# Optimization experiments

Hardware: AMD Instinct MI355X
Metric: run time of the kernel (lower is better)

Reference implementation:

```python
import jax, jax.numpy as jnp
import numpy as np

N, M, D, O = 16384, 4096, 256, 256

def setup_inputs() -> dict:
    key = jax.random.key(0)
    k1, k2, k3, k4, k5, k6, k7 = jax.random.split(key, 7)
    H_fine = jax.random.normal(k1, (N, D), dtype=jnp.float32)
    H_coarse = jax.random.normal(k2, (M, D), dtype=jnp.float32)
    inter_channel_adj = jax.random.randint(k3, (N, M), 0, 2).astype(jnp.float32)
    # attention = nn.Linear(2D, 1): weight vector [2D], bias scalar
    wa = jax.random.normal(k4, (2 * D,), dtype=jnp.float32) * (1.0 / np.sqrt(2 * D))
    ba = jax.random.normal(k5, (1,), dtype=jnp.float32) * 0.01
    # transform = nn.Linear(D, O), xavier_uniform weight
    lim = np.sqrt(6.0 / (D + O)).astype(np.float32)
    Wt = jax.random.uniform(k6, (O, D), minval=-lim, maxval=lim, dtype=jnp.float32)
    bt = jax.random.normal(k7, (O,), dtype=jnp.float32) * 0.01
    return {"H_fine": H_fine, "H_coarse": H_coarse,
            "inter_channel_adj": inter_channel_adj,
            "wa": wa, "ba": ba, "Wt": Wt, "bt": bt}

def reference(H_fine, H_coarse, inter_channel_adj, wa, ba, Wt, bt):
    d = H_fine.shape[-1]
    # additive attention: score_ij = [hf_i ; hc_j] . wa + b
    # = hf_i . wa[:d] + hc_j . wa[d:] + b  (avoids [N,M,2D] concat)
    sf = H_fine @ wa[:d]            # [N]
    sc = H_coarse @ wa[d:]          # [M]
    scores = sf[:, None] + sc[None, :] + ba[0]        # [N, M]
    masked = scores * inter_channel_adj               # [N, M]
    weights = jax.nn.softmax(masked, axis=-1)         # [N, M]
    attn_out = weights @ H_coarse                     # [N, D]
    attn_out = attn_out + H_fine                      # add_self=True
    out = attn_out @ Wt.T + bt                        # [N, O]
    return jax.nn.relu(out)
```

## Files before the change

kernel.cpp:

```cpp
#include <hip/hip_runtime.h>
#include <hip/hip_fp16.h>
#include <stdint.h>

#define N_ 16384
#define M_ 4096
#define D_ 256
#define O_ 256

#define WS_T    0
#define WS_U    65536
#define WS_R    81920
#define WS_WTP  98304
#define WS_BP   229376

typedef float  f32x4  __attribute__((ext_vector_type(4)));
typedef _Float16 half8 __attribute__((ext_vector_type(8)));

__device__ __forceinline__ unsigned short f2h(float f) {
  __half h = __float2half(f);
  unsigned short u;
  __builtin_memcpy(&u, &h, 2);
  return u;
}
__device__ __forceinline__ uint32_t hpack(float a, float b) {
  __half2 h = __floats2half2_rn(a, b);
  uint32_t u;
  __builtin_memcpy(&u, &h, 4);
  return u;
}

__global__ __launch_bounds__(256) void prep_kernel(
    const float* __restrict__ Hf, const float* __restrict__ Hc,
    const float* __restrict__ wa, const float* __restrict__ ba,
    const float* __restrict__ Wt, float* __restrict__ tv,
    float* __restrict__ uv, unsigned short* __restrict__ BP,
    unsigned short* __restrict__ WtP, float* __restrict__ Rv) {
  __shared__ float tile[64][65];
  __shared__ float red[4][64];
  int b = blockIdx.x;
  int t = threadIdx.x;
  if (b < 5120) {
    int wv = t >> 6, lane = t & 63;
    const float* X; const float* w; const float* bias; float* outv; int row;
    if (b < 4096) { X = Hf; w = wa;      bias = ba;      outv = tv; row = b * 4 + wv; }
    else          { X = Hc; w = wa + D_; bias = nullptr; outv = uv; row = (b - 4096) * 4 + wv; }
    const float4* x4 = (const float4*)(X + (size_t)row * D_);
    const float4* w4 = (const float4*)w;
    float4 xa = x4[lane], wa4 = w4[lane];
    float s = xa.x * wa4.x + xa.y * wa4.y + xa.z * wa4.z + xa.w * wa4.w;
#pragma unroll
    for (int off = 32; off > 0; off >>= 1) s += __shfl_xor(s, off);
    if (lane == 0) outv[row] = expf(s + (bias ? bias[0] : 0.0f));
  } else if (b < 5376) {
    int bb = b - 5120;
    int bk = bb >> 2;
    int bc = bb & 3;
    int k0 = bk * 64, col0 = bc * 64;
    int lane = t & 63, wv = t >> 6;
    int m = lane & 15, q = lane >> 4;
    float colsum = 0.0f;
#pragma unroll
    for (int i = 0; i < 16; ++i) {
      int e = t + 256 * i;
      int kk = e >> 6, cc = e & 63;
      float v = Hc[(size_t)(k0 + kk) * D_ + col0 + cc];
      tile[kk][cc] = v;
      colsum += v;
    }
    red[wv][t & 63] = colsum;
    __syncthreads();
    if (t < 64)
      atomicAdd(&Rv[col0 + t], red[0][t] + red[1][t] + red[2][t] + red[3][t]);
#pragma unroll
    for (int t8 = 0; t8 < 2; ++t8) {
      int tile_id = t8 * 4 + wv;
      int sub = tile_id >> 2, g = tile_id & 3;
      int kgg = bk * 2 + sub;
      int cgg = bc * 4 + g;
      unsigned short v8[8];
#pragma unroll
      for (int j = 0; j < 8; ++j)
        v8[j] = f2h(tile[sub * 32 + q * 8 + j][g * 16 + m]);
      *(uint4*)(BP + ((size_t)(kgg * 16 + cgg) * 64 + lane) * 8) = *(uint4*)v8;
    }
  } else {
    int tt = (b - 5376) * 256 + t;
    int lane = tt & 63, cg = (tt >> 6) & 15, kg = tt >> 10;
    int m = lane & 15, q = lane >> 4;
    const float* src = Wt + (size_t)(cg * 16 + m) * D_ + kg * 32 + q * 8;
    float4 w0 = *(const float4*)src, w1 = *(const float4*)(src + 4);
    unsigned short v8[8];
    v8[0] = f2h(w0.x); v8[1] = f2h(w0.y); v8[2] = f2h(w0.z); v8[3] = f2h(w0.w);
    v8[4] = f2h(w1.x); v8[5] = f2h(w1.y); v8[6] = f2h(w1.z); v8[7] = f2h(w1.w);
    *(uint4*)(WtP + (size_t)tt * 8) = *(uint4*)v8;
  }
}

__device__ __forceinline__ half8 frag_f16(uint32_t bits, __half2 th,
                                          const __half2* up, __half2 mone) {
  union { half8 h; uint32_t u[4]; } r;
#pragma unroll
  for (int p = 0; p < 4; ++p) {
    __half2 v = __hfma2(th, up[p], mone);
    uint32_t c;
    __builtin_memcpy(&c, &v, 4);
    uint32_t mlo = (uint32_t)((int32_t)(bits << (31 - 2 * p)) >> 31);
    uint32_t mhi = (uint32_t)((int32_t)(bits << (30 - 2 * p)) >> 31);
    r.u[p] = c & ((mlo & 0x0000FFFFu) | (mhi & 0xFFFF0000u));
  }
  return r.h;
}

#define LOADS(KB)                                                             \
  _Pragma("unroll")                                                           \
  for (int cc = 0; cc < 4; ++cc) {                                            \
    na0[cc] = ar[(size_t)0 * M_ + (KB) + cc * 64 + lane];                     \
    na1[cc] = ar[(size_t)1 * M_ + (KB) + cc * 64 + lane];                     \
    na2[cc] = ar[(size_t)2 * M_ + (KB) + cc * 64 + lane];                     \
    na3[cc] = ar[(size_t)3 * M_ + (KB) + cc * 64 + lane];                     \
  }

#define TAIL(BUF, KB)                                                         \
  {                                                                           \
    unsigned long long bal0[4], bal1[4], bal2[4], bal3[4];                    \
    _Pragma("unroll")                                                         \
    for (int cc = 0; cc < 4; ++cc) {                                          \
      float uvv = u_lds[(KB) + cc * 64 + lane];                               \
      bal0[cc] = __ballot(na0[cc] != 0.0f);                                   \
      bal1[cc] = __ballot(na1[cc] != 0.0f);                                   \
      bal2[cc] = __ballot(na2[cc] != 0.0f);                                   \
      bal3[cc] = __ballot(na3[cc] != 0.0f);                                   \
      su[0] = fmaf(na0[cc], uvv, su[0]);                                      \
      su[1] = fmaf(na1[cc], uvv, su[1]);                                      \
      su[2] = fmaf(na2[cc], uvv, su[2]);                                      \
      su[3] = fmaf(na3[cc], uvv, su[3]);                                      \
    }                                                                         \
    sc[0] += (na0[0] + na0[1]) + (na0[2] + na0[3]);                           \
    sc[1] += (na1[0] + na1[1]) + (na1[2] + na1[3]);                           \
    sc[2] += (na2[0] + na2[1]) + (na2[2] + na2[3]);                           \
    sc[3] += (na3[0] + na3[1]) + (na3[2] + na3[3]);                           \
    if (lane < 32) {                                                          \
      int rowsel = lane >> 3, ccs = (lane >> 1) & 3, hi = lane & 1;           \
      unsigned long long v0 = ccs == 0 ? bal0[0] : ccs == 1 ? bal0[1] : ccs == 2 ? bal0[2] : bal0[3]; \
      unsigned long long v1 = ccs == 0 ? bal1[0] : ccs == 1 ? bal1[1] : ccs == 2 ? bal1[2] : bal1[3]; \
      unsigned long long v2 = ccs == 0 ? bal2[0] : ccs == 1 ? bal2[1] : ccs == 2 ? bal2[2] : bal2[3]; \
      unsigned long long v3 = ccs == 0 ? bal3[0] : ccs == 1 ? bal3[1] : ccs == 2 ? bal3[2] : bal3[3]; \
      unsigned long long v = rowsel == 0 ? v0 : rowsel == 1 ? v1 : rowsel == 2 ? v2 : v3; \
      bits_lds[BUF][w * 4 + rowsel][ccs * 2 + hi] =                           \
          hi ? (unsigned int)(v >> 32) : (unsigned int)v;                     \
    }                                                                         \
  }

#define COMPUTE(C, BUF)                                                       \
  _Pragma("unroll")                                                           \
  for (int kk = 0; kk < 4; ++kk) {                                            \
    int kgc = ks * 4 + kk, kg = (C) * 8 + kgc;                                \
    uint32_t b32 = bits_lds[BUF][rt * 16 + m][kgc];                           \
    uint4 uu = *(const uint4*)&u_h2[kg * 16 + q * 4];                         \
    const unsigned short* bp = BP + ((size_t)(kg * 16 + cgh * 8)) * 512 + (size_t)lane * 8; \
    half8 bf0 = *(const half8*)(bp);                                          \
    half8 bf1 = *(const half8*)(bp + 512);                                    \
    half8 bf2 = *(const half8*)(bp + 1024);                                   \
    half8 bf3 = *(const half8*)(bp + 1536);                                   \
    half8 bf4 = *(const half8*)(bp + 2048);                                   \
    half8 bf5 = *(const half8*)(bp + 2560);                                   \
    half8 bf6 = *(const half8*)(bp + 3072);                                   \
    half8 bf7 = *(const half8*)(bp + 3584);                                   \
    __half2 up[4];                                                            \
    __builtin_memcpy(up, &uu, 16);                                            \
    half8 af = frag_f16((b32 >> sh) & 0xffu, th, up, mone);                   \
    acc[0] = __builtin_amdgcn_mfma_f32_16x16x32_f16(af, bf0, acc[0], 0, 0, 0); \
    acc[1] = __builtin_amdgcn_mfma_f32_16x16x32_f16(af, bf1, acc[1], 0, 0, 0); \
    acc[2] = __builtin_amdgcn_mfma_f32_16x16x32_f16(af, bf2, acc[2], 0, 0, 0); \
    acc[3] = __builtin_amdgcn_mfma_f32_16x16x32_f16(af, bf3, acc[3], 0, 0, 0); \
    acc[4] = __builtin_amdgcn_mfma_f32_16x16x32_f16(af, bf4, acc[4], 0, 0, 0); \
    acc[5] = __builtin_amdgcn_mfma_f32_16x16x32_f16(af, bf5, acc[5], 0, 0, 0); \
    acc[6] = __builtin_amdgcn_mfma_f32_16x16x32_f16(af, bf6, acc[6], 0, 0, 0); \
    acc[7] = __builtin_amdgcn_mfma_f32_16x16x32_f16(af, bf7, acc[7], 0, 0, 0); \
  }

__global__ __launch_bounds__(512, 4) void mega_kernel(
    const float* __restrict__ adj, const unsigned short* __restrict__ BP,
    const float* __restrict__ tv, const float* __restrict__ uv,
    const float* __restrict__ Rv, const float* __restrict__ Hf,
    const unsigned short* __restrict__ WtP, const float* __restrict__ bt,
    float* __restrict__ out) {
  __shared__ __align__(16) char smem[60288];
  unsigned int (*bits_lds)[32][9] = (unsigned int (*)[32][9])(smem);
  float* u_lds = (float*)(smem + 2304);
  uint32_t* u_h2 = (uint32_t*)(smem + 18688);
  float (*Cred)[260] = (float (*)[260])(smem + 26880);
  float* Lsum_lds = (float*)(smem + 60160);
  unsigned short (*attn)[264] = (unsigned short (*)[264])(smem);

  int tid = threadIdx.x;
  int w = tid >> 6, lane = tid & 63;
  int q = lane >> 4, m = lane & 15;
  int rt = w & 1, cgh = (w >> 1) & 1, ks = w >> 2;
  int sh = q * 8;
  int i0 = blockIdx.x * 32;

  const float* ar = adj + ((size_t)i0 + w * 4) * M_;
  float su[4] = {0.f, 0.f, 0.f, 0.f}, sc[4] = {0.f, 0.f, 0.f, 0.f};
  float na0[4], na1[4], na2[4], na3[4];

  LOADS(0)

  for (int i = tid; i < M_ / 2; i += 512) {
    float2 u2 = *(const float2*)(uv + 2 * i);
    u_lds[2 * i] = u2.x; u_lds[2 * i + 1] = u2.y;
    u_h2[i] = hpack(u2.x, u2.y);
  }

  __half2 th = __float2half2_rn(tv[i0 + rt * 16 + m]);
  const __half2 mone = __float2half2_rn(-1.0f);

  f32x4 acc[8];
#pragma unroll
  for (int n = 0; n < 8; ++n) acc[n] = (f32x4){0.f, 0.f, 0.f, 0.f};

  __syncthreads();
  TAIL(0, 0)
  __syncthreads();

#pragma unroll 1
  for (int c = 0; c < 16; ++c) {
    if (c < 15) { LOADS((c + 1) * 256) }
    COMPUTE(c, c & 1)
    if (c < 15) { TAIL((c + 1) & 1, (c + 1) * 256) }
    __syncthreads();
  }

#pragma unroll
  for (int off = 32; off > 0; off >>= 1) {
    su[0] += __shfl_xor(su[0], off); sc[0] += __shfl_xor(sc[0], off);
    su[1] += __shfl_xor(su[1], off); sc[1] += __shfl_xor(sc[1], off);
    su[2] += __shfl_xor(su[2], off); sc[2] += __shfl_xor(sc[2], off);
    su[3] += __shfl_xor(su[3], off); sc[3] += __shfl_xor(sc[3], off);
  }
  if (lane == 0) {
#pragma unroll
    for (int j = 0; j < 4; ++j)
      Lsum_lds[w * 4 + j] = tv[i0 + w * 4 + j] * su[j] - sc[j];
  }

#pragma unroll
  for (int s4 = 0; s4 < 2; ++s4) {
    if (ks == s4) {
#pragma unroll
      for (int g = 0; g < 8; ++g) {
        int col = (cgh * 8 + g) * 16 + m;
#pragma unroll
        for (int r = 0; r < 4; ++r) {
          int rl = rt * 16 + q * 4 + r;
          if (s4 == 0) Cred[rl][col] = acc[g][r];
          else         Cred[rl][col] += acc[g][r];
        }
      }
    }
    __syncthreads();
  }

  {
    int row = tid >> 4;
    int c0 = (tid & 15) * 16;
    size_t grow = (size_t)i0 + row;
    float invL = 1.0f / (Lsum_lds[row] + (float)M_);
    const float* hfp = Hf + grow * D_ + c0;
    const float* rvp = Rv + c0;
    const float* crp = &Cred[row][c0];
#pragma unroll
    for (int g = 0; g < 4; ++g) {
      float4 cv = *(const float4*)(crp + g * 4);
      float4 rv = *(const float4*)(rvp + g * 4);
      float4 hv = *(const float4*)(hfp + g * 4);
      float v0 = fmaf(cv.x + rv.x, invL, hv.x);
      float v1 = fmaf(cv.y + rv.y, invL, hv.y);
      float v2 = fmaf(cv.z + rv.z, invL, hv.z);
      float v3 = fmaf(cv.w + rv.w, invL, hv.w);
      *(uint32_t*)&attn[row][c0 + g * 4]     = hpack(v0, v1);
      *(uint32_t*)&attn[row][c0 + g * 4 + 2] = hpack(v2, v3);
    }
  }
  __syncthreads();

  {
    int rt2 = w & 1, cq = w >> 1;
    f32x4 facc[4];
#pragma unroll
    for (int n = 0; n < 4; ++n) facc[n] = (f32x4){0.f, 0.f, 0.f, 0.f};
    const unsigned short* wwave = WtP + (size_t)(cq * 4) * 512 + (size_t)lane * 8;
#pragma unroll
    for (int kf = 0; kf < 8; ++kf) {
      half8 af = *(const half8*)&attn[rt2 * 16 + m][kf * 32 + q * 8];
#pragma unroll
      for (int n = 0; n < 4; ++n) {
        half8 bf = *(const half8*)(wwave + ((size_t)kf * 16 + n) * 512);
        facc[n] = __builtin_amdgcn_mfma_f32_16x16x32_f16(af, bf, facc[n], 0, 0, 0);
      }
    }
#pragma unroll
    for (int n = 0; n < 4; ++n) {
      int col = cq * 64 + n * 16 + m;
      float b = bt[col];
#pragma unroll
      for (int r = 0; r < 4; ++r) {
        size_t row = (size_t)i0 + rt2 * 16 + q * 4 + r;
        out[row * O_ + col] = fmaxf(facc[n][r] + b, 0.0f);
      }
    }
  }
}

extern "C" void kernel_launch(void* const* d_in, const int* in_sizes, int n_in,
                              void* d_out, int out_size, void* d_ws, size_t ws_size,
                              hipStream_t stream) {
  const float* Hf  = (const float*)d_in[0];
  const float* Hc  = (const float*)d_in[1];
  const float* adj = (const float*)d_in[2];
  const float* wa  = (const float*)d_in[3];
  const float* ba  = (const float*)d_in[4];
  const float* Wt  = (const float*)d_in[5];
  const float* bt  = (const float*)d_in[6];
  float* out = (float*)d_out;

  char* ws = (char*)d_ws;
  float* tv   = (float*)(ws + WS_T);
  float* uv   = (float*)(ws + WS_U);
  float* Rv   = (float*)(ws + WS_R);
  unsigned short* WtP = (unsigned short*)(ws + WS_WTP);
  unsigned short* BP  = (unsigned short*)(ws + WS_BP);

  hipMemsetAsync(Rv, 0, D_ * sizeof(float), stream);

  prep_kernel<<<5408, 256, 0, stream>>>(Hf, Hc, wa, ba, Wt, tv, uv, BP, WtP, Rv);
  mega_kernel<<<512, 512, 0, stream>>>(adj, BP, tv, uv, Rv, Hf, WtP, bt, out);
}
```

Measured before the change: 430.9 us.

## Stage adjacency as fp16 tiles in LDS and split MFMA work by output columns

Replaces the ballot-bitmask encoding of the adjacency with direct fp16 staging of adjacency tiles in LDS, loaded as float4 per thread. The A fragment becomes an elementwise product of the adjacency and (t*u-1). Each wave now owns 32 output columns across all 32 rows over the full K range, so the cross-wave Cred reduction and its extra barriers go away and the epilogue works straight from the accumulators. The cost is more LDS traffic per chunk, with two A-fragment builds per k-step, and each B fragment now feeds only two MFMAs.

```diff
diff --git a/kernel.cpp b/kernel.cpp
--- a/kernel.cpp
+++ b/kernel.cpp
@@ -96,87 +96,60 @@
   }
 }
 
-__device__ __forceinline__ half8 frag_f16(uint32_t bits, __half2 th,
-                                          const __half2* up, __half2 mone) {
-  union { half8 h; uint32_t u[4]; } r;
-#pragma unroll
-  for (int p = 0; p < 4; ++p) {
-    __half2 v = __hfma2(th, up[p], mone);
-    uint32_t c;
-    __builtin_memcpy(&c, &v, 4);
-    uint32_t mlo = (uint32_t)((int32_t)(bits << (31 - 2 * p)) >> 31);
-    uint32_t mhi = (uint32_t)((int32_t)(bits << (30 - 2 * p)) >> 31);
-    r.u[p] = c & ((mlo & 0x0000FFFFu) | (mhi & 0xFFFF0000u));
-  }
-  return r.h;
+__device__ __forceinline__ half8 buildA(half8 a, __half2 th,
+                                        const __half2* up, __half2 mone) {
+  uint32_t ai[4], ro[4];
+  __builtin_memcpy(ai, &a, 16);
+#pragma unroll
+  for (int k = 0; k < 4; ++k) {
+    __half2 w2 = __hfma2(th, up[k], mone);
+    __half2 av;
+    __builtin_memcpy(&av, &ai[k], 4);
+    __half2 r = __hmul2(av, w2);
+    __builtin_memcpy(&ro[k], &r, 4);
+  }
+  half8 res;
+  __builtin_memcpy(&res, ro, 16);
+  return res;
 }
 
 #define LOADS(KB)                                                             \
   _Pragma("unroll")                                                           \
-  for (int cc = 0; cc < 4; ++cc) {                                            \
-    na0[cc] = ar[(size_t)0 * M_ + (KB) + cc * 64 + lane];                     \
-    na1[cc] = ar[(size_t)1 * M_ + (KB) + cc * 64 + lane];                     \
-    na2[cc] = ar[(size_t)2 * M_ + (KB) + cc * 64 + lane];                     \
-    na3[cc] = ar[(size_t)3 * M_ + (KB) + cc * 64 + lane];                     \
-  }
+  for (int p = 0; p < 4; ++p)                                                 \
+    na[p] = *(const float4*)(arow + (KB) + p * 64 + t15 * 4);
 
 #define TAIL(BUF, KB)                                                         \
-  {                                                                           \
-    unsigned long long bal0[4], bal1[4], bal2[4], bal3[4];                    \
-    _Pragma("unroll")                                                         \
-    for (int cc = 0; cc < 4; ++cc) {                                          \
-      float uvv = u_lds[(KB) + cc * 64 + lane];                               \
-      bal0[cc] = __ballot(na0[cc] != 0.0f);                                   \
-      bal1[cc] = __ballot(na1[cc] != 0.0f);                                   \
-      bal2[cc] = __ballot(na2[cc] != 0.0f);                                   \
-      bal3[cc] = __ballot(na3[cc] != 0.0f);                                   \
-      su[0] = fmaf(na0[cc], uvv, su[0]);                                      \
-      su[1] = fmaf(na1[cc], uvv, su[1]);                                      \
-      su[2] = fmaf(na2[cc], uvv, su[2]);                                      \
-      su[3] = fmaf(na3[cc], uvv, su[3]);                                      \
-    }                                                                         \
-    sc[0] += (na0[0] + na0[1]) + (na0[2] + na0[3]);                           \
-    sc[1] += (na1[0] + na1[1]) + (na1[2] + na1[3]);                           \
-    sc[2] += (na2[0] + na2[1]) + (na2[2] + na2[3]);                           \
-    sc[3] += (na3[0] + na3[1]) + (na3[2] + na3[3]);                           \
-    if (lane < 32) {                                                          \
-      int rowsel = lane >> 3, ccs = (lane >> 1) & 3, hi = lane & 1;           \
-      unsigned long long v0 = ccs == 0 ? bal0[0] : ccs == 1 ? bal0[1] : ccs == 2 ? bal0[2] : bal0[3]; \
-      unsigned long long v1 = ccs == 0 ? bal1[0] : ccs == 1 ? bal1[1] : ccs == 2 ? bal1[2] : bal1[3]; \
-      unsigned long long v2 = ccs == 0 ? bal2[0] : ccs == 1 ? bal2[1] : ccs == 2 ? bal2[2] : bal2[3]; \
-      unsigned long long v3 = ccs == 0 ? bal3[0] : ccs == 1 ? bal3[1] : ccs == 2 ? bal3[2] : bal3[3]; \
-      unsigned long long v = rowsel == 0 ? v0 : rowsel == 1 ? v1 : rowsel == 2 ? v2 : v3; \
-      bits_lds[BUF][w * 4 + rowsel][ccs * 2 + hi] =                           \
-          hi ? (unsigned int)(v >> 32) : (unsigned int)v;                     \
-    }                                                                         \
+  _Pragma("unroll")                                                           \
+  for (int p = 0; p < 4; ++p) {                                               \
+    int col = (KB) + p * 64 + t15 * 4;                                        \
+    float4 u4 = *(const float4*)&u_lds[col];                                  \
+    su = fmaf(na[p].x, u4.x, su); su = fmaf(na[p].y, u4.y, su);               \
+    su = fmaf(na[p].z, u4.z, su); su = fmaf(na[p].w, u4.w, su);               \
+    sc += (na[p].x + na[p].y) + (na[p].z + na[p].w);                          \
+    uint2 hv;                                                                 \
+    hv.x = hpack(na[p].x, na[p].y);                                           \
+    hv.y = hpack(na[p].z, na[p].w);                                           \
+    *(uint2*)&A_lds[BUF][srow][p * 64 + t15 * 4] = hv;                        \
   }
 
 #define COMPUTE(C, BUF)                                                       \
   _Pragma("unroll")                                                           \
-  for (int kk = 0; kk < 4; ++kk) {                                            \
-    int kgc = ks * 4 + kk, kg = (C) * 8 + kgc;                                \
-    uint32_t b32 = bits_lds[BUF][rt * 16 + m][kgc];                           \
-    uint4 uu = *(const uint4*)&u_h2[kg * 16 + q * 4];                         \
-    const unsigned short* bp = BP + ((size_t)(kg * 16 + cgh * 8)) * 512 + (size_t)lane * 8; \
+  for (int kgl = 0; kgl < 8; ++kgl) {                                         \
+    int kg = (C) * 8 + kgl;                                                   \
+    const unsigned short* bp = BP + ((size_t)(kg * 16 + w * 2)) * 512 + (size_t)lane * 8; \
     half8 bf0 = *(const half8*)(bp);                                          \
     half8 bf1 = *(const half8*)(bp + 512);                                    \
-    half8 bf2 = *(const half8*)(bp + 1024);                                   \
-    half8 bf3 = *(const half8*)(bp + 1536);                                   \
-    half8 bf4 = *(const half8*)(bp + 2048);                                   \
-    half8 bf5 = *(const half8*)(bp + 2560);                                   \
-    half8 bf6 = *(const half8*)(bp + 3072);                                   \
-    half8 bf7 = *(const half8*)(bp + 3584);                                   \
+    uint4 uu = *(const uint4*)&u_h2[kg * 16 + q * 4];                         \
     __half2 up[4];                                                            \
     __builtin_memcpy(up, &uu, 16);                                            \
-    half8 af = frag_f16((b32 >> sh) & 0xffu, th, up, mone);                   \
-    acc[0] = __builtin_amdgcn_mfma_f32_16x16x32_f16(af, bf0, acc[0], 0, 0, 0); \
-    acc[1] = __builtin_amdgcn_mfma_f32_16x16x32_f16(af, bf1, acc[1], 0, 0, 0); \
-    acc[2] = __builtin_amdgcn_mfma_f32_16x16x32_f16(af, bf2, acc[2], 0, 0, 0); \
-    acc[3] = __builtin_amdgcn_mfma_f32_16x16x32_f16(af, bf3, acc[3], 0, 0, 0); \
-    acc[4] = __builtin_amdgcn_mfma_f32_16x16x32_f16(af, bf4, acc[4], 0, 0, 0); \
-    acc[5] = __builtin_amdgcn_mfma_f32_16x16x32_f16(af, bf5, acc[5], 0, 0, 0); \
-    acc[6] = __builtin_amdgcn_mfma_f32_16x16x32_f16(af, bf6, acc[6], 0, 0, 0); \
-    acc[7] = __builtin_amdgcn_mfma_f32_16x16x32_f16(af, bf7, acc[7], 0, 0, 0); \
+    half8 a0 = *(const half8*)&A_lds[BUF][m][kgl * 32 + q * 8];               \
+    half8 a1 = *(const half8*)&A_lds[BUF][16 + m][kgl * 32 + q * 8];          \
+    half8 af0 = buildA(a0, th0, up, mone);                                    \
+    half8 af1 = buildA(a1, th1, up, mone);                                    \
+    acc[0][0] = __builtin_amdgcn_mfma_f32_16x16x32_f16(af0, bf0, acc[0][0], 0, 0, 0); \
+    acc[0][1] = __builtin_amdgcn_mfma_f32_16x16x32_f16(af0, bf1, acc[0][1], 0, 0, 0); \
+    acc[1][0] = __builtin_amdgcn_mfma_f32_16x16x32_f16(af1, bf0, acc[1][0], 0, 0, 0); \
+    acc[1][1] = __builtin_amdgcn_mfma_f32_16x16x32_f16(af1, bf1, acc[1][1], 0, 0, 0); \
   }
 
 __global__ __launch_bounds__(512, 4) void mega_kernel(
@@ -185,24 +158,22 @@
     const float* __restrict__ Rv, const float* __restrict__ Hf,
     const unsigned short* __restrict__ WtP, const float* __restrict__ bt,
     float* __restrict__ out) {
-  __shared__ __align__(16) char smem[60288];
-  unsigned int (*bits_lds)[32][9] = (unsigned int (*)[32][9])(smem);
-  float* u_lds = (float*)(smem + 2304);
-  uint32_t* u_h2 = (uint32_t*)(smem + 18688);
-  float (*Cred)[260] = (float (*)[260])(smem + 26880);
-  float* Lsum_lds = (float*)(smem + 60160);
+  __shared__ __align__(16) char smem[59520];
+  unsigned short (*A_lds)[32][272] = (unsigned short (*)[32][272])(smem);
+  float* u_lds = (float*)(smem + 34816);
+  uint32_t* u_h2 = (uint32_t*)(smem + 51200);
+  float* Lsum_lds = (float*)(smem + 59392);
   unsigned short (*attn)[264] = (unsigned short (*)[264])(smem);
 
   int tid = threadIdx.x;
   int w = tid >> 6, lane = tid & 63;
   int q = lane >> 4, m = lane & 15;
-  int rt = w & 1, cgh = (w >> 1) & 1, ks = w >> 2;
-  int sh = q * 8;
+  int srow = tid >> 4, t15 = tid & 15;
   int i0 = blockIdx.x * 32;
 
-  const float* ar = adj + ((size_t)i0 + w * 4) * M_;
-  float su[4] = {0.f, 0.f, 0.f, 0.f}, sc[4] = {0.f, 0.f, 0.f, 0.f};
-  float na0[4], na1[4], na2[4], na3[4];
+  const float* arow = adj + ((size_t)i0 + srow) * M_;
+  float su = 0.f, sc = 0.f;
+  float4 na[4];
 
   LOADS(0)
 
@@ -212,12 +183,15 @@
     u_h2[i] = hpack(u2.x, u2.y);
   }
 
-  __half2 th = __float2half2_rn(tv[i0 + rt * 16 + m]);
+  __half2 th0 = __float2half2_rn(tv[i0 + m]);
+  __half2 th1 = __float2half2_rn(tv[i0 + 16 + m]);
   const __half2 mone = __float2half2_rn(-1.0f);
 
-  f32x4 acc[8];
-#pragma unroll
-  for (int n = 0; n < 8; ++n) acc[n] = (f32x4){0.f, 0.f, 0.f, 0.f};
+  f32x4 acc[2][2];
+#pragma unroll
+  for (int s = 0; s < 2; ++s)
+#pragma unroll
+    for (int n = 0; n < 2; ++n) acc[s][n] = (f32x4){0.f, 0.f, 0.f, 0.f};
 
   __syncthreads();
   TAIL(0, 0)
@@ -232,55 +206,29 @@
   }
 
 #pragma unroll
-  for (int off = 32; off > 0; off >>= 1) {
-    su[0] += __shfl_xor(su[0], off); sc[0] += __shfl_xor(sc[0], off);
-    su[1] += __shfl_xor(su[1], off); sc[1] += __shfl_xor(sc[1], off);
-    su[2] += __shfl_xor(su[2], off); sc[2] += __shfl_xor(sc[2], off);
-    su[3] += __shfl_xor(su[3], off); sc[3] += __shfl_xor(sc[3], off);
-  }
-  if (lane == 0) {
-#pragma unroll
-    for (int j = 0; j < 4; ++j)
-      Lsum_lds[w * 4 + j] = tv[i0 + w * 4 + j] * su[j] - sc[j];
-  }
-
-#pragma unroll
-  for (int s4 = 0; s4 < 2; ++s4) {
-    if (ks == s4) {
-#pragma unroll
-      for (int g = 0; g < 8; ++g) {
-        int col = (cgh * 8 + g) * 16 + m;
-#pragma unroll
-        for (int r = 0; r < 4; ++r) {
-          int rl = rt * 16 + q * 4 + r;
-          if (s4 == 0) Cred[rl][col] = acc[g][r];
-          else         Cred[rl][col] += acc[g][r];
-        }
+  for (int off = 1; off < 16; off <<= 1) {
+    su += __shfl_xor(su, off);
+    sc += __shfl_xor(sc, off);
+  }
+  if (t15 == 0)
+    Lsum_lds[srow] = tv[i0 + srow] * su - sc;
+  __syncthreads();
+
+  {
+    float rv0 = Rv[w * 32 + m];
+    float rv1 = Rv[w * 32 + 16 + m];
+#pragma unroll
+    for (int rt = 0; rt < 2; ++rt)
+#pragma unroll
+      for (int r = 0; r < 4; ++r) {
+        int row = rt * 16 + q * 4 + r;
+        float invL = 1.0f / (Lsum_lds[row] + (float)M_);
+        size_t grow = (size_t)i0 + row;
+        float h0 = Hf[grow * D_ + w * 32 + m];
+        float h1 = Hf[grow * D_ + w * 32 + 16 + m];
+        attn[row][w * 32 + m]      = f2h(fmaf(acc[rt][0][r] + rv0, invL, h0));
+        attn[row][w * 32 + 16 + m] = f2h(fmaf(acc[rt][1][r] + rv1, invL, h1));
       }
-    }
-    __syncthreads();
-  }
-
-  {
-    int row = tid >> 4;
-    int c0 = (tid & 15) * 16;
-    size_t grow = (size_t)i0 + row;
-    float invL = 1.0f / (Lsum_lds[row] + (float)M_);
-    const float* hfp = Hf + grow * D_ + c0;
-    const float* rvp = Rv + c0;
-    const float* crp = &Cred[row][c0];
-#pragma unroll
-    for (int g = 0; g < 4; ++g) {
-      float4 cv = *(const float4*)(crp + g * 4);
-      float4 rv = *(const float4*)(rvp + g * 4);
-      float4 hv = *(const float4*)(hfp + g * 4);
-      float v0 = fmaf(cv.x + rv.x, invL, hv.x);
-      float v1 = fmaf(cv.y + rv.y, invL, hv.y);
-      float v2 = fmaf(cv.z + rv.z, invL, hv.z);
-      float v3 = fmaf(cv.w + rv.w, invL, hv.w);
-      *(uint32_t*)&attn[row][c0 + g * 4]     = hpack(v0, v1);
-      *(uint32_t*)&attn[row][c0 + g * 4 + 2] = hpack(v2, v3);
-    }
   }
   __syncthreads();
 
```

New measurement: 440.9 us. 2.3% more time.
